# Performance work log

Measured on AMD Instinct MI355X. Metric: run time of the kernel, lower is better.

Reference implementation:

```python
import jax, jax.numpy as jnp
import numpy as np

N = 50000
IN_C, HID_C, OUT_C = 128, 64, 32
E = 800000
NEG_SLOPE = 0.2


def setup_inputs() -> dict:
    key = jax.random.key(0)
    ks = jax.random.split(key, 8)
    x = jax.random.normal(ks[0], (N, IN_C), dtype=jnp.float32)
    edge_index = jax.random.randint(ks[1], (2, E), 0, N, dtype=jnp.int64)
    # GATConv params (heads=1): lin weight, att_src/att_dst vectors, bias
    sc = 1.0 / np.sqrt(IN_C)
    W = jax.random.uniform(ks[2], (IN_C, HID_C), jnp.float32, -sc, sc)
    att_src = jax.random.normal(ks[3], (HID_C,), jnp.float32) * (1.0 / np.sqrt(HID_C))
    att_dst = jax.random.normal(ks[4], (HID_C,), jnp.float32) * (1.0 / np.sqrt(HID_C))
    bias_conv = jnp.zeros((HID_C,), jnp.float32)
    sl = 1.0 / np.sqrt(HID_C)
    W_lin = jax.random.uniform(ks[5], (HID_C, OUT_C), jnp.float32, -sl, sl)
    b_lin = jax.random.uniform(ks[6], (OUT_C,), jnp.float32, -sl, sl)
    return {"x": x, "edge_index": edge_index, "W": W, "att_src": att_src,
            "att_dst": att_dst, "bias_conv": bias_conv, "W_lin": W_lin, "b_lin": b_lin}


def reference(x, edge_index, W, att_src, att_dst, bias_conv, W_lin, b_lin):
    n = x.shape[0]
    h = x @ W  # [N, HID]
    # add self-loops (PyG GATConv default add_self_loops=True)
    loop = jnp.arange(n, dtype=edge_index.dtype)
    src = jnp.concatenate([edge_index[0], loop])  # [E+N]
    dst = jnp.concatenate([edge_index[1], loop])
    a_src = h @ att_src  # [N]
    a_dst = h @ att_dst
    e = jax.nn.leaky_relu(a_src[src] + a_dst[dst], NEG_SLOPE)  # [E+N]
    # segment softmax over incoming edges per destination node
    m = jax.ops.segment_max(e, dst, num_segments=n)
    e = jnp.exp(e - m[dst])
    denom = jax.ops.segment_sum(e, dst, num_segments=n)
    alpha = e / (denom[dst] + 1e-16)
    msg = alpha[:, None] * h[src]  # [E+N, HID]
    out = jax.ops.segment_sum(msg, dst, num_segments=n) + bias_conv
    out = jax.nn.relu(out)
    return out @ W_lin + b_lin
```

## Files before the change

kernel.cpp:

```cpp
#include <hip/hip_runtime.h>
#include <hip/hip_bf16.h>

#define IN_C  128
#define HID_C 64
#define OUT_C 32
#define NEG_SLOPE 0.2f
#define EPB1    4096
#define BUCKETW 64
#define RCAP    1536
#define NBKT    1024
#define CSTRIDE 16
#define XS_LD   136

typedef short bf16x8 __attribute__((ext_vector_type(8)));
typedef float f32x4  __attribute__((ext_vector_type(4)));

__device__ __forceinline__ unsigned short f2bf(float f) {
    __hip_bfloat16 h = __float2bfloat16(f);
    return *(unsigned short*)&h;
}
__device__ __forceinline__ float bflo(unsigned int u) {
    return __uint_as_float(u << 16);
}
__device__ __forceinline__ float bfhi(unsigned int u) {
    return __uint_as_float(u & 0xffff0000u);
}

__global__ __launch_bounds__(512) void gemm_bin1_kernel(
    const float* __restrict__ x, const float* __restrict__ W,
    const float* __restrict__ att_src, const float* __restrict__ att_dst,
    __hip_bfloat16* __restrict__ hb,
    float* __restrict__ a_src, float* __restrict__ a_dst,
    const int* __restrict__ ei, int E,
    int* __restrict__ bcur, unsigned* __restrict__ bucketbuf,
    int ngemm, int n_nodes)
{
    __shared__ __align__(16) unsigned char smem[52224];
    const int t = threadIdx.x;

    if ((int)blockIdx.x < ngemm) {
        unsigned short* xs = (unsigned short*)smem;
        unsigned short* wt = (unsigned short*)(smem + 34816);
        const int wv   = t >> 6;
        const int lane = t & 63;
        const int m16  = lane & 15;
        const int quad = lane >> 4;
        const int node0 = blockIdx.x * 128;
        const int nrows = min(128, n_nodes - node0);

        {
            const float4* xg = (const float4*)(x + (long)node0 * IN_C);
#pragma unroll
            for (int i = t; i < 4096; i += 512) {
                const int row = i >> 5;
                const int c4  = i & 31;
                float4 v = (row < nrows) ? xg[i] : make_float4(0.f, 0.f, 0.f, 0.f);
                ushort4 u;
                u.x = f2bf(v.x); u.y = f2bf(v.y);
                u.z = f2bf(v.z); u.w = f2bf(v.w);
                *(ushort4*)(xs + row * XS_LD + c4 * 4) = u;
            }
        }
        {
#pragma unroll
            for (int i = t; i < 2048; i += 512) {
                const int k  = i >> 4;
                const int n0 = (i & 15) * 4;
                const float4 v = *(const float4*)(W + k * HID_C + n0);
                wt[(n0 + 0) * XS_LD + k] = f2bf(v.x);
                wt[(n0 + 1) * XS_LD + k] = f2bf(v.y);
                wt[(n0 + 2) * XS_LD + k] = f2bf(v.z);
                wt[(n0 + 3) * XS_LD + k] = f2bf(v.w);
            }
        }
        __syncthreads();

        const int myrow0 = wv * 16;
        bf16x8 A[4];
#pragma unroll
        for (int k0 = 0; k0 < 4; ++k0)
            A[k0] = *(const bf16x8*)(xs + (myrow0 + m16) * XS_LD + k0 * 32 + quad * 8);

        f32x4 C[4];
#pragma unroll
        for (int c = 0; c < 4; ++c) {
            C[c] = (f32x4){0.f, 0.f, 0.f, 0.f};
#pragma unroll
            for (int k0 = 0; k0 < 4; ++k0) {
                const bf16x8 B = *(const bf16x8*)(wt + (c * 16 + m16) * XS_LD + k0 * 32 + quad * 8);
                C[c] = __builtin_amdgcn_mfma_f32_16x16x32_bf16(A[k0], B, C[c], 0, 0, 0);
            }
        }

#pragma unroll
        for (int c = 0; c < 4; ++c) {
#pragma unroll
            for (int r = 0; r < 4; ++r)
                xs[(myrow0 + quad * 4 + r) * XS_LD + c * 16 + m16] = f2bf(C[c][r]);
        }

        {
            float ps[4] = {0.f, 0.f, 0.f, 0.f};
            float pd[4] = {0.f, 0.f, 0.f, 0.f};
#pragma unroll
            for (int c = 0; c < 4; ++c) {
                const float av = att_src[c * 16 + m16];
                const float dv = att_dst[c * 16 + m16];
#pragma unroll
                for (int r = 0; r < 4; ++r) {
                    ps[r] = fmaf(C[c][r], av, ps[r]);
                    pd[r] = fmaf(C[c][r], dv, pd[r]);
                }
            }
#pragma unroll
            for (int off = 1; off <= 8; off <<= 1) {
#pragma unroll
                for (int r = 0; r < 4; ++r) {
                    ps[r] += __shfl_xor(ps[r], off, 64);
                    pd[r] += __shfl_xor(pd[r], off, 64);
                }
            }
            if (m16 == 0) {
#pragma unroll
                for (int r = 0; r < 4; ++r) {
                    const int row = myrow0 + quad * 4 + r;
                    if (row < nrows) {
                        a_src[node0 + row] = ps[r];
                        a_dst[node0 + row] = pd[r];
                    }
                }
            }
        }
        __syncthreads();

        {
#pragma unroll
            for (int i = t; i < 1024; i += 512) {
                const int row = i >> 3;
                const int c8  = (i & 7) * 8;
                if (row < nrows) {
                    const uint4 v = *(const uint4*)(xs + row * XS_LD + c8);
                    *(uint4*)((unsigned short*)hb + (long)(node0 + row) * HID_C + c8) = v;
                }
            }
        }
    } else {
        unsigned* stage = (unsigned*)smem;
        int* excl = (int*)(smem + 16384);
        int* cur  = (int*)(smem + 20480);
        int* gpos = (int*)(smem + 24576);
        int* wsum = (int*)(smem + 28672);

        const int base = (blockIdx.x - ngemm) * EPB1;
        const int nedge = min(EPB1, E - base);
        const int lane = t & 63, wv = t >> 6;

        for (int i = t; i < NBKT; i += 512) excl[i] = 0;
        __syncthreads();

        for (int i = t; i < nedge; i += 512)
            atomicAdd(&excl[ei[E + base + i] >> 6], 1);
        __syncthreads();

        {
            const int b0 = t * 2;
            const int c0 = excl[b0], c1 = excl[b0 + 1];
            const int tsum = c0 + c1;
            int incl = tsum;
#pragma unroll
            for (int off = 1; off <= 32; off <<= 1) {
                int u = __shfl_up(incl, off, 64);
                if (lane >= off) incl += u;
            }
            if (lane == 63) wsum[wv] = incl;
            __syncthreads();
            int wbase = 0;
#pragma unroll
            for (int w = 0; w < 8; ++w) wbase += (w < wv) ? wsum[w] : 0;
            int run = wbase + (incl - tsum);
            excl[b0]     = run; cur[b0]     = run; run += c0;
            excl[b0 + 1] = run; cur[b0 + 1] = run;
        }
        __syncthreads();

        for (int i = t; i < nedge; i += 512) {
            const int s = ei[base + i];
            const int d = ei[E + base + i];
            const int b = d >> 6;
            const int pos = atomicAdd(&cur[b], 1);
            stage[pos] = (unsigned)s | ((unsigned)(d & 63) << 16)
                         | ((unsigned)b << 22);
        }
        __syncthreads();

        for (int b = t; b < NBKT; b += 512) {
            const int c = cur[b] - excl[b];
            gpos[b] = (c > 0) ? atomicAdd(&bcur[b * CSTRIDE], c) : 0;
        }
        __syncthreads();

        for (int i = t; i < nedge; i += 512) {
            const unsigned r = stage[i];
            const int b = r >> 22;
            const int dp = gpos[b] + (i - excl[b]);
            if (dp < RCAP) bucketbuf[(long)b * RCAP + dp] = r & 0x3FFFFFu;
        }
    }
}

__global__ __launch_bounds__(512) void bucket_agg_kernel(
    const unsigned* __restrict__ bucketbuf, const int* __restrict__ bcursor,
    const __hip_bfloat16* __restrict__ hb,
    const float* __restrict__ a_src, const float* __restrict__ a_dst,
    const float* __restrict__ bias_conv,
    const float* __restrict__ W_lin, const float* __restrict__ b_lin,
    float* __restrict__ out, int n_nodes)
{
    __shared__ unsigned srtL[RCAP];
    __shared__ int cntd[BUCKETW];
    __shared__ int rp[BUCKETW + 1];
    __shared__ int curd[BUCKETW];

    const int t  = threadIdx.x;
    const int q  = blockIdx.x;
    const int d0 = q * BUCKETW;
    const int dmax = min(BUCKETW, n_nodes - d0);
    const int tot  = min(bcursor[q * CSTRIDE], RCAP);
    const int wv = t >> 6, lane = t & 63, g8 = lane >> 3, l = lane & 7;

    if (t < BUCKETW) cntd[t] = 0;
    __syncthreads();

    const unsigned* gsrc = bucketbuf + (long)q * RCAP;

    const int i0 = t, i1 = t + 512, i2 = t + 1024;
    const bool v0 = i0 < tot, v1 = i1 < tot, v2 = i2 < tot;
    const unsigned rr0 = v0 ? gsrc[i0] : 0u;
    const unsigned rr1 = v1 ? gsrc[i1] : 0u;
    const unsigned rr2 = v2 ? gsrc[i2] : 0u;

    if (v0) atomicAdd(&cntd[(rr0 >> 16) & 63], 1);
    if (v1) atomicAdd(&cntd[(rr1 >> 16) & 63], 1);
    if (v2) atomicAdd(&cntd[(rr2 >> 16) & 63], 1);
    __syncthreads();

    if (t < 64) {
        int c = cntd[t], incl = c;
#pragma unroll
        for (int off = 1; off <= 32; off <<= 1) {
            int u = __shfl_up(incl, off, 64);
            if (t >= off) incl += u;
        }
        rp[t] = incl - c;
        curd[t] = incl - c;
        if (t == 63) rp[64] = incl;
    }
    __syncthreads();

    if (v0) { const int pos = atomicAdd(&curd[(rr0 >> 16) & 63], 1); srtL[pos] = rr0; }
    if (v1) { const int pos = atomicAdd(&curd[(rr1 >> 16) & 63], 1); srtL[pos] = rr1; }
    if (v2) { const int pos = atomicAdd(&curd[(rr2 >> 16) & 63], 1); srtL[pos] = rr2; }
    __syncthreads();

    float Wr[8][4];
#pragma unroll
    for (int kc = 0; kc < 8; ++kc)
#pragma unroll
        for (int kj = 0; kj < 4; ++kj)
            Wr[kc][kj] = W_lin[(l * 8 + kc) * OUT_C + g8 * 4 + kj];
    float biasR[8];
#pragma unroll
    for (int kc = 0; kc < 8; ++kc) biasR[kc] = bias_conv[l * 8 + kc];
    float blinR[4];
#pragma unroll
    for (int kj = 0; kj < 4; ++kj) blinR[kj] = b_lin[g8 * 4 + kj];

    const unsigned short* hbs = (const unsigned short*)hb;

    for (int dloc = wv; dloc < dmax; dloc += 8) {
        const int d = d0 + dloc;
        const float ad = a_dst[d];
        float A[8] = {0.f,0.f,0.f,0.f,0.f,0.f,0.f,0.f};
        float den = 0.f;
        if (g8 == 0) {
            float e = a_src[d] + ad;
            e = (e >= 0.f) ? e : NEG_SLOPE * e;
            const float ws = __expf(e);
            const uint4 hv = *(const uint4*)(hbs + (long)d * HID_C + l * 8);
            den = ws;
            A[0] = ws * bflo(hv.x); A[1] = ws * bfhi(hv.x);
            A[2] = ws * bflo(hv.y); A[3] = ws * bfhi(hv.y);
            A[4] = ws * bflo(hv.z); A[5] = ws * bfhi(hv.z);
            A[6] = ws * bflo(hv.w); A[7] = ws * bfhi(hv.w);
        }
        const int beg = rp[dloc], fin = rp[dloc + 1];
        for (int j = beg + g8; j < fin; j += 16) {
            const int  j1   = j + 8;
            const bool has1 = j1 < fin;
            const unsigned r0 = srtL[j];
            const unsigned r1 = srtL[has1 ? j1 : j];
            const int   s0 = r0 & 0xFFFF;
            const int   s1 = r1 & 0xFFFF;
            const float as0 = a_src[s0];
            const float as1 = a_src[s1];
            const uint4 h0 = *(const uint4*)(hbs + (long)s0 * HID_C + l * 8);
            const uint4 h1 = *(const uint4*)(hbs + (long)s1 * HID_C + l * 8);
            float e0 = as0 + ad; e0 = (e0 >= 0.f) ? e0 : NEG_SLOPE * e0;
            float e1 = as1 + ad; e1 = (e1 >= 0.f) ? e1 : NEG_SLOPE * e1;
            const float w0 = __expf(e0);
            const float w1 = has1 ? __expf(e1) : 0.f;
            den += w0 + w1;
            A[0] = fmaf(w0, bflo(h0.x), A[0]); A[1] = fmaf(w0, bfhi(h0.x), A[1]);
            A[2] = fmaf(w0, bflo(h0.y), A[2]); A[3] = fmaf(w0, bfhi(h0.y), A[3]);
            A[4] = fmaf(w0, bflo(h0.z), A[4]); A[5] = fmaf(w0, bfhi(h0.z), A[5]);
            A[6] = fmaf(w0, bflo(h0.w), A[6]); A[7] = fmaf(w0, bfhi(h0.w), A[7]);
            A[0] = fmaf(w1, bflo(h1.x), A[0]); A[1] = fmaf(w1, bfhi(h1.x), A[1]);
            A[2] = fmaf(w1, bflo(h1.y), A[2]); A[3] = fmaf(w1, bfhi(h1.y), A[3]);
            A[4] = fmaf(w1, bflo(h1.z), A[4]); A[5] = fmaf(w1, bfhi(h1.z), A[5]);
            A[6] = fmaf(w1, bflo(h1.w), A[6]); A[7] = fmaf(w1, bfhi(h1.w), A[7]);
        }
#pragma unroll
        for (int off = 8; off <= 32; off <<= 1) {
#pragma unroll
            for (int k = 0; k < 8; ++k) A[k] += __shfl_xor(A[k], off, 64);
            den += __shfl_xor(den, off, 64);
        }
        const float rd = 1.0f / (den + 1e-16f);
        float p0 = 0.f, p1 = 0.f, p2 = 0.f, p3 = 0.f;
#pragma unroll
        for (int kc = 0; kc < 8; ++kc) {
            float vv = fmaf(A[kc], rd, biasR[kc]);
            vv = vv > 0.f ? vv : 0.f;
            p0 = fmaf(vv, Wr[kc][0], p0);
            p1 = fmaf(vv, Wr[kc][1], p1);
            p2 = fmaf(vv, Wr[kc][2], p2);
            p3 = fmaf(vv, Wr[kc][3], p3);
        }
#pragma unroll
        for (int off = 1; off <= 4; off <<= 1) {
            p0 += __shfl_xor(p0, off, 64);
            p1 += __shfl_xor(p1, off, 64);
            p2 += __shfl_xor(p2, off, 64);
            p3 += __shfl_xor(p3, off, 64);
        }
        if (l == 0) {
            float4 o = make_float4(p0 + blinR[0], p1 + blinR[1],
                                   p2 + blinR[2], p3 + blinR[3]);
            *(float4*)(out + (long)d * OUT_C + g8 * 4) = o;
        }
    }
}

extern "C" void kernel_launch(void* const* d_in, const int* in_sizes, int n_in,
                              void* d_out, int out_size, void* d_ws, size_t ws_size,
                              hipStream_t stream) {
    const float* x         = (const float*)d_in[0];
    const int*   ei        = (const int*)d_in[1];
    const float* W         = (const float*)d_in[2];
    const float* att_src   = (const float*)d_in[3];
    const float* att_dst   = (const float*)d_in[4];
    const float* bias_conv = (const float*)d_in[5];
    const float* W_lin     = (const float*)d_in[6];
    const float* b_lin     = (const float*)d_in[7];
    float*       out       = (float*)d_out;

    const int n_nodes = in_sizes[0] / IN_C;
    const int E       = in_sizes[1] / 2;
    const int B1   = (E + EPB1 - 1) / EPB1;
    const int Q    = (n_nodes + BUCKETW - 1) / BUCKETW;
    const int NG   = (n_nodes + 127) / 128;

    __hip_bfloat16* hb = (__hip_bfloat16*)d_ws;
    float* a_src   = (float*)(hb + (long)n_nodes * HID_C);
    float* a_dst   = a_src + n_nodes;
    int*   bcur    = (int*)(a_dst + n_nodes);
    unsigned* bucketbuf = (unsigned*)(bcur + (long)Q * CSTRIDE);

    hipMemsetAsync(bcur, 0, (size_t)Q * CSTRIDE * sizeof(int), stream);

    gemm_bin1_kernel<<<NG + B1, 512, 0, stream>>>(
        x, W, att_src, att_dst, hb, a_src, a_dst,
        ei, E, bcur, bucketbuf, NG, n_nodes);

    bucket_agg_kernel<<<Q, 512, 0, stream>>>(
        bucketbuf, bcur, hb, a_src, a_dst,
        bias_conv, W_lin, b_lin, out, n_nodes);
}
```

Before: 150.5 us.

## Fuse GEMM, binning and aggregation into one persistent kernel with grid barrier

Merges the two kernels into a single persistent kernel of 512 blocks. The blocks loop over GEMM and edge-binning work units, meet at a software grid barrier, then loop over aggregation buckets. Buckets now span 98 nodes instead of 64, giving 512 buckets, and each bucket record stores the full destination id. This removes a kernel launch and the gap between kernels. In exchange it relies on all 512 blocks being resident at once for the spin barrier, which includes a guard-break that could silently proceed, and it uses integer division by 98.

```diff
diff --git a/kernel.cpp b/kernel.cpp
--- a/kernel.cpp
+++ b/kernel.cpp
@@ -6,11 +6,12 @@
 #define OUT_C 32
 #define NEG_SLOPE 0.2f
 #define EPB1    4096
-#define BUCKETW 64
-#define RCAP    1536
-#define NBKT    1024
+#define BUCKETW 98
+#define RCAP    2048
+#define NBKT    512
 #define CSTRIDE 16
 #define XS_LD   136
+#define NBLK    512
 
 typedef short bf16x8 __attribute__((ext_vector_type(8)));
 typedef float f32x4  __attribute__((ext_vector_type(4)));
@@ -26,327 +27,355 @@
     return __uint_as_float(u & 0xffff0000u);
 }
 
-__global__ __launch_bounds__(512) void gemm_bin1_kernel(
+__device__ __forceinline__ void grid_barrier(int* ctr, int nb) {
+    __syncthreads();
+    __threadfence();
+    if (threadIdx.x == 0) {
+        atomicAdd(ctr, 1);
+        int guard = 0;
+        while (__hip_atomic_load(ctr, __ATOMIC_RELAXED,
+                                 __HIP_MEMORY_SCOPE_AGENT) < nb) {
+            __builtin_amdgcn_s_sleep(8);
+            if (++guard > (1 << 20)) break;
+        }
+    }
+    __syncthreads();
+    __threadfence();
+}
+
+__global__ __launch_bounds__(512, 4) void gat_fused(
     const float* __restrict__ x, const float* __restrict__ W,
     const float* __restrict__ att_src, const float* __restrict__ att_dst,
     __hip_bfloat16* __restrict__ hb,
     float* __restrict__ a_src, float* __restrict__ a_dst,
     const int* __restrict__ ei, int E,
-    int* __restrict__ bcur, unsigned* __restrict__ bucketbuf,
-    int ngemm, int n_nodes)
+    int* __restrict__ bar, int* __restrict__ bcur,
+    unsigned* __restrict__ bucketbuf,
+    const float* __restrict__ bias_conv,
+    const float* __restrict__ W_lin, const float* __restrict__ b_lin,
+    float* __restrict__ out,
+    int ngemm, int nbin, int nreg, int n_nodes)
 {
     __shared__ __align__(16) unsigned char smem[52224];
-    const int t = threadIdx.x;
-
-    if ((int)blockIdx.x < ngemm) {
-        unsigned short* xs = (unsigned short*)smem;
-        unsigned short* wt = (unsigned short*)(smem + 34816);
-        const int wv   = t >> 6;
-        const int lane = t & 63;
-        const int m16  = lane & 15;
-        const int quad = lane >> 4;
-        const int node0 = blockIdx.x * 128;
-        const int nrows = min(128, n_nodes - node0);
-
-        {
-            const float4* xg = (const float4*)(x + (long)node0 * IN_C);
-#pragma unroll
-            for (int i = t; i < 4096; i += 512) {
-                const int row = i >> 5;
-                const int c4  = i & 31;
-                float4 v = (row < nrows) ? xg[i] : make_float4(0.f, 0.f, 0.f, 0.f);
-                ushort4 u;
-                u.x = f2bf(v.x); u.y = f2bf(v.y);
-                u.z = f2bf(v.z); u.w = f2bf(v.w);
-                *(ushort4*)(xs + row * XS_LD + c4 * 4) = u;
-            }
-        }
-        {
-#pragma unroll
-            for (int i = t; i < 2048; i += 512) {
-                const int k  = i >> 4;
-                const int n0 = (i & 15) * 4;
-                const float4 v = *(const float4*)(W + k * HID_C + n0);
-                wt[(n0 + 0) * XS_LD + k] = f2bf(v.x);
-                wt[(n0 + 1) * XS_LD + k] = f2bf(v.y);
-                wt[(n0 + 2) * XS_LD + k] = f2bf(v.z);
-                wt[(n0 + 3) * XS_LD + k] = f2bf(v.w);
-            }
-        }
-        __syncthreads();
-
-        const int myrow0 = wv * 16;
-        bf16x8 A[4];
-#pragma unroll
-        for (int k0 = 0; k0 < 4; ++k0)
-            A[k0] = *(const bf16x8*)(xs + (myrow0 + m16) * XS_LD + k0 * 32 + quad * 8);
-
-        f32x4 C[4];
-#pragma unroll
-        for (int c = 0; c < 4; ++c) {
-            C[c] = (f32x4){0.f, 0.f, 0.f, 0.f};
-#pragma unroll
-            for (int k0 = 0; k0 < 4; ++k0) {
-                const bf16x8 B = *(const bf16x8*)(wt + (c * 16 + m16) * XS_LD + k0 * 32 + quad * 8);
-                C[c] = __builtin_amdgcn_mfma_f32_16x16x32_bf16(A[k0], B, C[c], 0, 0, 0);
-            }
-        }
-
-#pragma unroll
-        for (int c = 0; c < 4; ++c) {
-#pragma unroll
-            for (int r = 0; r < 4; ++r)
-                xs[(myrow0 + quad * 4 + r) * XS_LD + c * 16 + m16] = f2bf(C[c][r]);
-        }
-
-        {
-            float ps[4] = {0.f, 0.f, 0.f, 0.f};
-            float pd[4] = {0.f, 0.f, 0.f, 0.f};
+    const int t   = threadIdx.x;
+    const int bid = blockIdx.x;
+
+    for (int u = bid; u < ngemm + nbin; u += NBLK) {
+        if (u < ngemm) {
+            unsigned short* xs = (unsigned short*)smem;
+            unsigned short* wt = (unsigned short*)(smem + 34816);
+            const int wv   = t >> 6;
+            const int lane = t & 63;
+            const int m16  = lane & 15;
+            const int quad = lane >> 4;
+            const int node0 = u * 128;
+            const int nrows = min(128, n_nodes - node0);
+
+            __syncthreads();
+
+            {
+                const float4* xg = (const float4*)(x + (long)node0 * IN_C);
+#pragma unroll
+                for (int i = t; i < 4096; i += 512) {
+                    const int row = i >> 5;
+                    const int c4  = i & 31;
+                    float4 v = (row < nrows) ? xg[i] : make_float4(0.f, 0.f, 0.f, 0.f);
+                    ushort4 uu;
+                    uu.x = f2bf(v.x); uu.y = f2bf(v.y);
+                    uu.z = f2bf(v.z); uu.w = f2bf(v.w);
+                    *(ushort4*)(xs + row * XS_LD + c4 * 4) = uu;
+                }
+            }
+            {
+#pragma unroll
+                for (int i = t; i < 2048; i += 512) {
+                    const int k  = i >> 4;
+                    const int n0 = (i & 15) * 4;
+                    const float4 v = *(const float4*)(W + k * HID_C + n0);
+                    wt[(n0 + 0) * XS_LD + k] = f2bf(v.x);
+                    wt[(n0 + 1) * XS_LD + k] = f2bf(v.y);
+                    wt[(n0 + 2) * XS_LD + k] = f2bf(v.z);
+                    wt[(n0 + 3) * XS_LD + k] = f2bf(v.w);
+                }
+            }
+            __syncthreads();
+
+            const int myrow0 = wv * 16;
+            bf16x8 A[4];
+#pragma unroll
+            for (int k0 = 0; k0 < 4; ++k0)
+                A[k0] = *(const bf16x8*)(xs + (myrow0 + m16) * XS_LD + k0 * 32 + quad * 8);
+
+            f32x4 C[4];
 #pragma unroll
             for (int c = 0; c < 4; ++c) {
-                const float av = att_src[c * 16 + m16];
-                const float dv = att_dst[c * 16 + m16];
-#pragma unroll
-                for (int r = 0; r < 4; ++r) {
-                    ps[r] = fmaf(C[c][r], av, ps[r]);
-                    pd[r] = fmaf(C[c][r], dv, pd[r]);
-                }
-            }
-#pragma unroll
-            for (int off = 1; off <= 8; off <<= 1) {
-#pragma unroll
-                for (int r = 0; r < 4; ++r) {
-                    ps[r] += __shfl_xor(ps[r], off, 64);
-                    pd[r] += __shfl_xor(pd[r], off, 64);
-                }
-            }
-            if (m16 == 0) {
-#pragma unroll
-                for (int r = 0; r < 4; ++r) {
-                    const int row = myrow0 + quad * 4 + r;
+                C[c] = (f32x4){0.f, 0.f, 0.f, 0.f};
+#pragma unroll
+                for (int k0 = 0; k0 < 4; ++k0) {
+                    const bf16x8 B = *(const bf16x8*)(wt + (c * 16 + m16) * XS_LD + k0 * 32 + quad * 8);
+                    C[c] = __builtin_amdgcn_mfma_f32_16x16x32_bf16(A[k0], B, C[c], 0, 0, 0);
+                }
+            }
+
+#pragma unroll
+            for (int c = 0; c < 4; ++c) {
+#pragma unroll
+                for (int r = 0; r < 4; ++r)
+                    xs[(myrow0 + quad * 4 + r) * XS_LD + c * 16 + m16] = f2bf(C[c][r]);
+            }
+
+            {
+                float ps[4] = {0.f, 0.f, 0.f, 0.f};
+                float pd[4] = {0.f, 0.f, 0.f, 0.f};
+#pragma unroll
+                for (int c = 0; c < 4; ++c) {
+                    const float av = att_src[c * 16 + m16];
+                    const float dv = att_dst[c * 16 + m16];
+#pragma unroll
+                    for (int r = 0; r < 4; ++r) {
+                        ps[r] = fmaf(C[c][r], av, ps[r]);
+                        pd[r] = fmaf(C[c][r], dv, pd[r]);
+                    }
+                }
+#pragma unroll
+                for (int off = 1; off <= 8; off <<= 1) {
+#pragma unroll
+                    for (int r = 0; r < 4; ++r) {
+                        ps[r] += __shfl_xor(ps[r], off, 64);
+                        pd[r] += __shfl_xor(pd[r], off, 64);
+                    }
+                }
+                if (m16 == 0) {
+#pragma unroll
+                    for (int r = 0; r < 4; ++r) {
+                        const int row = myrow0 + quad * 4 + r;
+                        if (row < nrows) {
+                            a_src[node0 + row] = ps[r];
+                            a_dst[node0 + row] = pd[r];
+                        }
+                    }
+                }
+            }
+            __syncthreads();
+
+            {
+#pragma unroll
+                for (int i = t; i < 1024; i += 512) {
+                    const int row = i >> 3;
+                    const int c8  = (i & 7) * 8;
                     if (row < nrows) {
-                        a_src[node0 + row] = ps[r];
-                        a_dst[node0 + row] = pd[r];
+                        const uint4 v = *(const uint4*)(xs + row * XS_LD + c8);
+                        *(uint4*)((unsigned short*)hb + (long)(node0 + row) * HID_C + c8) = v;
                     }
                 }
             }
-        }
-        __syncthreads();
-
-        {
-#pragma unroll
-            for (int i = t; i < 1024; i += 512) {
-                const int row = i >> 3;
-                const int c8  = (i & 7) * 8;
-                if (row < nrows) {
-                    const uint4 v = *(const uint4*)(xs + row * XS_LD + c8);
-                    *(uint4*)((unsigned short*)hb + (long)(node0 + row) * HID_C + c8) = v;
-                }
-            }
-        }
-    } else {
-        unsigned* stage = (unsigned*)smem;
-        int* excl = (int*)(smem + 16384);
-        int* cur  = (int*)(smem + 20480);
-        int* gpos = (int*)(smem + 24576);
-        int* wsum = (int*)(smem + 28672);
-
-        const int base = (blockIdx.x - ngemm) * EPB1;
-        const int nedge = min(EPB1, E - base);
-        const int lane = t & 63, wv = t >> 6;
-
-        for (int i = t; i < NBKT; i += 512) excl[i] = 0;
-        __syncthreads();
-
-        for (int i = t; i < nedge; i += 512)
-            atomicAdd(&excl[ei[E + base + i] >> 6], 1);
-        __syncthreads();
-
-        {
-            const int b0 = t * 2;
-            const int c0 = excl[b0], c1 = excl[b0 + 1];
-            const int tsum = c0 + c1;
-            int incl = tsum;
-#pragma unroll
-            for (int off = 1; off <= 32; off <<= 1) {
-                int u = __shfl_up(incl, off, 64);
-                if (lane >= off) incl += u;
-            }
-            if (lane == 63) wsum[wv] = incl;
-            __syncthreads();
-            int wbase = 0;
-#pragma unroll
-            for (int w = 0; w < 8; ++w) wbase += (w < wv) ? wsum[w] : 0;
-            int run = wbase + (incl - tsum);
-            excl[b0]     = run; cur[b0]     = run; run += c0;
-            excl[b0 + 1] = run; cur[b0 + 1] = run;
-        }
-        __syncthreads();
-
-        for (int i = t; i < nedge; i += 512) {
-            const int s = ei[base + i];
-            const int d = ei[E + base + i];
-            const int b = d >> 6;
-            const int pos = atomicAdd(&cur[b], 1);
-            stage[pos] = (unsigned)s | ((unsigned)(d & 63) << 16)
-                         | ((unsigned)b << 22);
-        }
-        __syncthreads();
-
-        for (int b = t; b < NBKT; b += 512) {
-            const int c = cur[b] - excl[b];
-            gpos[b] = (c > 0) ? atomicAdd(&bcur[b * CSTRIDE], c) : 0;
-        }
-        __syncthreads();
-
-        for (int i = t; i < nedge; i += 512) {
-            const unsigned r = stage[i];
-            const int b = r >> 22;
-            const int dp = gpos[b] + (i - excl[b]);
-            if (dp < RCAP) bucketbuf[(long)b * RCAP + dp] = r & 0x3FFFFFu;
+        } else {
+            unsigned* stage = (unsigned*)smem;
+            int* excl = (int*)(smem + 16384);
+            int* cur  = (int*)(smem + 18432);
+            int* gpos = (int*)(smem + 20480);
+            int* wsum = (int*)(smem + 22528);
+
+            const int base = (u - ngemm) * EPB1;
+            const int nedge = min(EPB1, E - base);
+            const int lane = t & 63, wv = t >> 6;
+
+            __syncthreads();
+
+            excl[t] = 0;
+            __syncthreads();
+
+            for (int i = t; i < nedge; i += 512)
+                atomicAdd(&excl[(unsigned)ei[E + base + i] / 98u], 1);
+            __syncthreads();
+
+            {
+                const int c = excl[t];
+                int incl = c;
+#pragma unroll
+                for (int off = 1; off <= 32; off <<= 1) {
+                    int uu = __shfl_up(incl, off, 64);
+                    if (lane >= off) incl += uu;
+                }
+                if (lane == 63) wsum[wv] = incl;
+                __syncthreads();
+                int wbase = 0;
+#pragma unroll
+                for (int w = 0; w < 8; ++w) wbase += (w < wv) ? wsum[w] : 0;
+                const int e = wbase + incl - c;
+                excl[t] = e; cur[t] = e;
+            }
+            __syncthreads();
+
+            for (int i = t; i < nedge; i += 512) {
+                const int s = ei[base + i];
+                const int d = ei[E + base + i];
+                const int b = (unsigned)d / 98u;
+                const int pos = atomicAdd(&cur[b], 1);
+                stage[pos] = (unsigned)s | ((unsigned)d << 16);
+            }
+            __syncthreads();
+
+            {
+                const int c = cur[t] - excl[t];
+                gpos[t] = (c > 0) ? atomicAdd(&bcur[t * CSTRIDE], c) : 0;
+            }
+            __syncthreads();
+
+            for (int i = t; i < nedge; i += 512) {
+                const unsigned r = stage[i];
+                const int b = (r >> 16) / 98u;
+                const int dp = gpos[b] + (i - excl[b]);
+                if (dp < RCAP) bucketbuf[(long)b * RCAP + dp] = r;
+            }
         }
     }
-}
-
-__global__ __launch_bounds__(512) void bucket_agg_kernel(
-    const unsigned* __restrict__ bucketbuf, const int* __restrict__ bcursor,
-    const __hip_bfloat16* __restrict__ hb,
-    const float* __restrict__ a_src, const float* __restrict__ a_dst,
-    const float* __restrict__ bias_conv,
-    const float* __restrict__ W_lin, const float* __restrict__ b_lin,
-    float* __restrict__ out, int n_nodes)
-{
-    __shared__ unsigned srtL[RCAP];
-    __shared__ int cntd[BUCKETW];
-    __shared__ int rp[BUCKETW + 1];
-    __shared__ int curd[BUCKETW];
-
-    const int t  = threadIdx.x;
-    const int q  = blockIdx.x;
-    const int d0 = q * BUCKETW;
-    const int dmax = min(BUCKETW, n_nodes - d0);
-    const int tot  = min(bcursor[q * CSTRIDE], RCAP);
-    const int wv = t >> 6, lane = t & 63, g8 = lane >> 3, l = lane & 7;
-
-    if (t < BUCKETW) cntd[t] = 0;
-    __syncthreads();
-
-    const unsigned* gsrc = bucketbuf + (long)q * RCAP;
-
-    const int i0 = t, i1 = t + 512, i2 = t + 1024;
-    const bool v0 = i0 < tot, v1 = i1 < tot, v2 = i2 < tot;
-    const unsigned rr0 = v0 ? gsrc[i0] : 0u;
-    const unsigned rr1 = v1 ? gsrc[i1] : 0u;
-    const unsigned rr2 = v2 ? gsrc[i2] : 0u;
-
-    if (v0) atomicAdd(&cntd[(rr0 >> 16) & 63], 1);
-    if (v1) atomicAdd(&cntd[(rr1 >> 16) & 63], 1);
-    if (v2) atomicAdd(&cntd[(rr2 >> 16) & 63], 1);
-    __syncthreads();
-
-    if (t < 64) {
-        int c = cntd[t], incl = c;
-#pragma unroll
-        for (int off = 1; off <= 32; off <<= 1) {
-            int u = __shfl_up(incl, off, 64);
-            if (t >= off) incl += u;
+
+    grid_barrier(bar, NBLK);
+
+    unsigned* srtL = (unsigned*)smem;
+    int* cntd = (int*)(smem + 8192);
+    int* rp   = (int*)(smem + 8584);
+    int* curd = (int*)(smem + 8980);
+
+    for (int q = bid; q < nreg; q += NBLK) {
+        const int d0 = q * BUCKETW;
+        const int dmax = min(BUCKETW, n_nodes - d0);
+        const int tot  = min(bcur[q * CSTRIDE], RCAP);
+        const int wv = t >> 6, lane = t & 63, g8 = lane >> 3, l = lane & 7;
+
+        __syncthreads();
+        if (t < BUCKETW) cntd[t] = 0;
+        __syncthreads();
+
+        const unsigned* gsrc = bucketbuf + (long)q * RCAP;
+
+        const int i0 = t, i1 = t + 512, i2 = t + 1024, i3 = t + 1536;
+        const bool v0 = i0 < tot, v1 = i1 < tot, v2 = i2 < tot, v3 = i3 < tot;
+        const unsigned rr0 = v0 ? gsrc[i0] : 0u;
+        const unsigned rr1 = v1 ? gsrc[i1] : 0u;
+        const unsigned rr2 = v2 ? gsrc[i2] : 0u;
+        const unsigned rr3 = v3 ? gsrc[i3] : 0u;
+
+        if (v0) atomicAdd(&cntd[(int)(rr0 >> 16) - d0], 1);
+        if (v1) atomicAdd(&cntd[(int)(rr1 >> 16) - d0], 1);
+        if (v2) atomicAdd(&cntd[(int)(rr2 >> 16) - d0], 1);
+        if (v3) atomicAdd(&cntd[(int)(rr3 >> 16) - d0], 1);
+        __syncthreads();
+
+        if (t < 64) {
+            int c = cntd[t], incl = c;
+#pragma unroll
+            for (int off = 1; off <= 32; off <<= 1) {
+                int uu = __shfl_up(incl, off, 64);
+                if (t >= off) incl += uu;
+            }
+            rp[t] = incl - c;
+            curd[t] = incl - c;
+            if (t == 63) rp[64] = incl;
         }
-        rp[t] = incl - c;
-        curd[t] = incl - c;
-        if (t == 63) rp[64] = incl;
-    }
-    __syncthreads();
-
-    if (v0) { const int pos = atomicAdd(&curd[(rr0 >> 16) & 63], 1); srtL[pos] = rr0; }
-    if (v1) { const int pos = atomicAdd(&curd[(rr1 >> 16) & 63], 1); srtL[pos] = rr1; }
-    if (v2) { const int pos = atomicAdd(&curd[(rr2 >> 16) & 63], 1); srtL[pos] = rr2; }
-    __syncthreads();
-
-    float Wr[8][4];
-#pragma unroll
-    for (int kc = 0; kc < 8; ++kc)
-#pragma unroll
-        for (int kj = 0; kj < 4; ++kj)
-            Wr[kc][kj] = W_lin[(l * 8 + kc) * OUT_C + g8 * 4 + kj];
-    float biasR[8];
-#pragma unroll
-    for (int kc = 0; kc < 8; ++kc) biasR[kc] = bias_conv[l * 8 + kc];
-    float blinR[4];
-#pragma unroll
-    for (int kj = 0; kj < 4; ++kj) blinR[kj] = b_lin[g8 * 4 + kj];
-
-    const unsigned short* hbs = (const unsigned short*)hb;
-
-    for (int dloc = wv; dloc < dmax; dloc += 8) {
-        const int d = d0 + dloc;
-        const float ad = a_dst[d];
-        float A[8] = {0.f,0.f,0.f,0.f,0.f,0.f,0.f,0.f};
-        float den = 0.f;
-        if (g8 == 0) {
-            float e = a_src[d] + ad;
-            e = (e >= 0.f) ? e : NEG_SLOPE * e;
-            const float ws = __expf(e);
-            const uint4 hv = *(const uint4*)(hbs + (long)d * HID_C + l * 8);
-            den = ws;
-            A[0] = ws * bflo(hv.x); A[1] = ws * bfhi(hv.x);
-            A[2] = ws * bflo(hv.y); A[3] = ws * bfhi(hv.y);
-            A[4] = ws * bflo(hv.z); A[5] = ws * bfhi(hv.z);
-            A[6] = ws * bflo(hv.w); A[7] = ws * bfhi(hv.w);
+        __syncthreads();
+        if (t == 0) {
+            int run = rp[64];
+            for (int k = 64; k < BUCKETW; ++k) {
+                rp[k] = run; curd[k] = run; run += cntd[k];
+            }
+            rp[BUCKETW] = run;
         }
-        const int beg = rp[dloc], fin = rp[dloc + 1];
-        for (int j = beg + g8; j < fin; j += 16) {
-            const int  j1   = j + 8;
-            const bool has1 = j1 < fin;
-            const unsigned r0 = srtL[j];
-            const unsigned r1 = srtL[has1 ? j1 : j];
-            const int   s0 = r0 & 0xFFFF;
-            const int   s1 = r1 & 0xFFFF;
-            const float as0 = a_src[s0];
-            const float as1 = a_src[s1];
-            const uint4 h0 = *(const uint4*)(hbs + (long)s0 * HID_C + l * 8);
-            const uint4 h1 = *(const uint4*)(hbs + (long)s1 * HID_C + l * 8);
-            float e0 = as0 + ad; e0 = (e0 >= 0.f) ? e0 : NEG_SLOPE * e0;
-            float e1 = as1 + ad; e1 = (e1 >= 0.f) ? e1 : NEG_SLOPE * e1;
-            const float w0 = __expf(e0);
-            const float w1 = has1 ? __expf(e1) : 0.f;
-            den += w0 + w1;
-            A[0] = fmaf(w0, bflo(h0.x), A[0]); A[1] = fmaf(w0, bfhi(h0.x), A[1]);
-            A[2] = fmaf(w0, bflo(h0.y), A[2]); A[3] = fmaf(w0, bfhi(h0.y), A[3]);
-            A[4] = fmaf(w0, bflo(h0.z), A[4]); A[5] = fmaf(w0, bfhi(h0.z), A[5]);
-            A[6] = fmaf(w0, bflo(h0.w), A[6]); A[7] = fmaf(w0, bfhi(h0.w), A[7]);
-            A[0] = fmaf(w1, bflo(h1.x), A[0]); A[1] = fmaf(w1, bfhi(h1.x), A[1]);
-            A[2] = fmaf(w1, bflo(h1.y), A[2]); A[3] = fmaf(w1, bfhi(h1.y), A[3]);
-            A[4] = fmaf(w1, bflo(h1.z), A[4]); A[5] = fmaf(w1, bfhi(h1.z), A[5]);
-            A[6] = fmaf(w1, bflo(h1.w), A[6]); A[7] = fmaf(w1, bfhi(h1.w), A[7]);
-        }
-#pragma unroll
-        for (int off = 8; off <= 32; off <<= 1) {
-#pragma unroll
-            for (int k = 0; k < 8; ++k) A[k] += __shfl_xor(A[k], off, 64);
-            den += __shfl_xor(den, off, 64);
-        }
-        const float rd = 1.0f / (den + 1e-16f);
-        float p0 = 0.f, p1 = 0.f, p2 = 0.f, p3 = 0.f;
-#pragma unroll
-        for (int kc = 0; kc < 8; ++kc) {
-            float vv = fmaf(A[kc], rd, biasR[kc]);
-            vv = vv > 0.f ? vv : 0.f;
-            p0 = fmaf(vv, Wr[kc][0], p0);
-            p1 = fmaf(vv, Wr[kc][1], p1);
-            p2 = fmaf(vv, Wr[kc][2], p2);
-            p3 = fmaf(vv, Wr[kc][3], p3);
-        }
-#pragma unroll
-        for (int off = 1; off <= 4; off <<= 1) {
-            p0 += __shfl_xor(p0, off, 64);
-            p1 += __shfl_xor(p1, off, 64);
-            p2 += __shfl_xor(p2, off, 64);
-            p3 += __shfl_xor(p3, off, 64);
-        }
-        if (l == 0) {
-            float4 o = make_float4(p0 + blinR[0], p1 + blinR[1],
-                                   p2 + blinR[2], p3 + blinR[3]);
-            *(float4*)(out + (long)d * OUT_C + g8 * 4) = o;
+        __syncthreads();
+
+        if (v0) { const int p = atomicAdd(&curd[(int)(rr0 >> 16) - d0], 1); srtL[p] = rr0; }
+        if (v1) { const int p = atomicAdd(&curd[(int)(rr1 >> 16) - d0], 1); srtL[p] = rr1; }
+        if (v2) { const int p = atomicAdd(&curd[(int)(rr2 >> 16) - d0], 1); srtL[p] = rr2; }
+        if (v3) { const int p = atomicAdd(&curd[(int)(rr3 >> 16) - d0], 1); srtL[p] = rr3; }
+        __syncthreads();
+
+        float Wr[8][4];
+#pragma unroll
+        for (int kc = 0; kc < 8; ++kc)
+#pragma unroll
+            for (int kj = 0; kj < 4; ++kj)
+                Wr[kc][kj] = W_lin[(l * 8 + kc) * OUT_C + g8 * 4 + kj];
+        float biasR[8];
+#pragma unroll
+        for (int kc = 0; kc < 8; ++kc) biasR[kc] = bias_conv[l * 8 + kc];
+        float blinR[4];
+#pragma unroll
+        for (int kj = 0; kj < 4; ++kj) blinR[kj] = b_lin[g8 * 4 + kj];
+
+        const unsigned short* hbs = (const unsigned short*)hb;
+
+        for (int dloc = wv; dloc < dmax; dloc += 8) {
+            const int d = d0 + dloc;
+            const float ad = a_dst[d];
+            float A[8] = {0.f,0.f,0.f,0.f,0.f,0.f,0.f,0.f};
+            float den = 0.f;
+            if (g8 == 0) {
+                float e = a_src[d] + ad;
+                e = (e >= 0.f) ? e : NEG_SLOPE * e;
+                const float ws = __expf(e);
+                const uint4 hv = *(const uint4*)(hbs + (long)d * HID_C + l * 8);
+                den = ws;
+                A[0] = ws * bflo(hv.x); A[1] = ws * bfhi(hv.x);
+                A[2] = ws * bflo(hv.y); A[3] = ws * bfhi(hv.y);
+                A[4] = ws * bflo(hv.z); A[5] = ws * bfhi(hv.z);
+                A[6] = ws * bflo(hv.w); A[7] = ws * bfhi(hv.w);
+            }
+            const int beg = rp[dloc], fin = rp[dloc + 1];
+            for (int j = beg + g8; j < fin; j += 16) {
+                const int  j1   = j + 8;
+                const bool has1 = j1 < fin;
+                const unsigned r0 = srtL[j];
+                const unsigned r1 = srtL[has1 ? j1 : j];
+                const int   s0 = r0 & 0xFFFF;
+                const int   s1 = r1 & 0xFFFF;
+                const float as0 = a_src[s0];
+                const float as1 = a_src[s1];
+                const uint4 h0 = *(const uint4*)(hbs + (long)s0 * HID_C + l * 8);
+                const uint4 h1 = *(const uint4*)(hbs + (long)s1 * HID_C + l * 8);
+                float e0 = as0 + ad; e0 = (e0 >= 0.f) ? e0 : NEG_SLOPE * e0;
+                float e1 = as1 + ad; e1 = (e1 >= 0.f) ? e1 : NEG_SLOPE * e1;
+                const float w0 = __expf(e0);
+                const float w1 = has1 ? __expf(e1) : 0.f;
+                den += w0 + w1;
+                A[0] = fmaf(w0, bflo(h0.x), A[0]); A[1] = fmaf(w0, bfhi(h0.x), A[1]);
+                A[2] = fmaf(w0, bflo(h0.y), A[2]); A[3] = fmaf(w0, bfhi(h0.y), A[3]);
+                A[4] = fmaf(w0, bflo(h0.z), A[4]); A[5] = fmaf(w0, bfhi(h0.z), A[5]);
+                A[6] = fmaf(w0, bflo(h0.w), A[6]); A[7] = fmaf(w0, bfhi(h0.w), A[7]);
+                A[0] = fmaf(w1, bflo(h1.x), A[0]); A[1] = fmaf(w1, bfhi(h1.x), A[1]);
+                A[2] = fmaf(w1, bflo(h1.y), A[2]); A[3] = fmaf(w1, bfhi(h1.y), A[3]);
+                A[4] = fmaf(w1, bflo(h1.z), A[4]); A[5] = fmaf(w1, bfhi(h1.z), A[5]);
+                A[6] = fmaf(w1, bflo(h1.w), A[6]); A[7] = fmaf(w1, bfhi(h1.w), A[7]);
+            }
+#pragma unroll
+            for (int off = 8; off <= 32; off <<= 1) {
+#pragma unroll
+                for (int k = 0; k < 8; ++k) A[k] += __shfl_xor(A[k], off, 64);
+                den += __shfl_xor(den, off, 64);
+            }
+            const float rd = 1.0f / (den + 1e-16f);
+            float p0 = 0.f, p1 = 0.f, p2 = 0.f, p3 = 0.f;
+#pragma unroll
+            for (int kc = 0; kc < 8; ++kc) {
+                float vv = fmaf(A[kc], rd, biasR[kc]);
+                vv = vv > 0.f ? vv : 0.f;
+                p0 = fmaf(vv, Wr[kc][0], p0);
+                p1 = fmaf(vv, Wr[kc][1], p1);
+                p2 = fmaf(vv, Wr[kc][2], p2);
+                p3 = fmaf(vv, Wr[kc][3], p3);
+            }
+#pragma unroll
+            for (int off = 1; off <= 4; off <<= 1) {
+                p0 += __shfl_xor(p0, off, 64);
+                p1 += __shfl_xor(p1, off, 64);
+                p2 += __shfl_xor(p2, off, 64);
+                p3 += __shfl_xor(p3, off, 64);
+            }
+            if (l == 0) {
+                float4 o = make_float4(p0 + blinR[0], p1 + blinR[1],
+                                       p2 + blinR[2], p3 + blinR[3]);
+                *(float4*)(out + (long)d * OUT_C + g8 * 4) = o;
+            }
         }
     }
 }
@@ -364,25 +393,25 @@
     const float* b_lin     = (const float*)d_in[7];
     float*       out       = (float*)d_out;
 
-    const int n_nodes = in_sizes[0] / IN_C;
-    const int E       = in_sizes[1] / 2;
-    const int B1   = (E + EPB1 - 1) / EPB1;
-    const int Q    = (n_nodes + BUCKETW - 1) / BUCKETW;
-    const int NG   = (n_nodes + 127) / 128;
+    int n_nodes = in_sizes[0] / IN_C;
+    int E       = in_sizes[1] / 2;
+    int nbin    = (E + EPB1 - 1) / EPB1;
+    int nreg    = (n_nodes + BUCKETW - 1) / BUCKETW;
+    int ngemm   = (n_nodes + 127) / 128;
 
     __hip_bfloat16* hb = (__hip_bfloat16*)d_ws;
     float* a_src   = (float*)(hb + (long)n_nodes * HID_C);
     float* a_dst   = a_src + n_nodes;
-    int*   bcur    = (int*)(a_dst + n_nodes);
-    unsigned* bucketbuf = (unsigned*)(bcur + (long)Q * CSTRIDE);
-
-    hipMemsetAsync(bcur, 0, (size_t)Q * CSTRIDE * sizeof(int), stream);
-
-    gemm_bin1_kernel<<<NG + B1, 512, 0, stream>>>(
+    int*   bar     = (int*)(a_dst + n_nodes);
+    int*   bcur    = bar + 16;
+    unsigned* bucketbuf = (unsigned*)(bcur + (long)nreg * CSTRIDE);
+
+    hipMemsetAsync(bar, 0, (size_t)(16 + (long)nreg * CSTRIDE) * sizeof(int),
+                   stream);
+
+    gat_fused<<<NBLK, 512, 0, stream>>>(
         x, W, att_src, att_dst, hb, a_src, a_dst,
-        ei, E, bcur, bucketbuf, NG, n_nodes);
-
-    bucket_agg_kernel<<<Q, 512, 0, stream>>>(
-        bucketbuf, bcur, hb, a_src, a_dst,
-        bias_conv, W_lin, b_lin, out, n_nodes);
-}
+        ei, E, bar, bcur, bucketbuf,
+        bias_conv, W_lin, b_lin, out,
+        ngemm, nbin, nreg, n_nodes);
+}
```

New measurement: 319.0 us. 2.12x slower.

## Precompute per-edge attention weights in a separate kernel before aggregation

Applied to the files above, without the earlier changes.

Adds a weight_kernel that computes exp(leaky_relu(a_src+a_dst)) for every bucketed edge and stores it in a new global buffer. The aggregation kernel then loads these weights, sorts them into shared memory alongside the edge records, and no longer does the a_src gather or the exp in its inner loop. This takes the dependent scalar gather and the transcendental off the critical path of the aggregation loop. In exchange it adds a kernel launch, an extra global write and read of the weights, and more shared memory per block, which may lower occupancy.

```diff
diff --git a/kernel.cpp b/kernel.cpp
--- a/kernel.cpp
+++ b/kernel.cpp
@@ -208,8 +208,37 @@
     }
 }
 
+__global__ __launch_bounds__(512) void weight_kernel(
+    const unsigned* __restrict__ bucketbuf, const int* __restrict__ bcursor,
+    const float* __restrict__ a_src, const float* __restrict__ a_dst,
+    float* __restrict__ wbuf)
+{
+    const int t = threadIdx.x;
+    const int q = blockIdx.x;
+    const int d0 = q * BUCKETW;
+    const int tot = min(bcursor[q * CSTRIDE], RCAP);
+    const unsigned* src = bucketbuf + (long)q * RCAP;
+    float* wdst = wbuf + (long)q * RCAP;
+
+    const int i0 = t, i1 = t + 512, i2 = t + 1024;
+    const bool v0 = i0 < tot, v1 = i1 < tot, v2 = i2 < tot;
+    const unsigned r0 = v0 ? src[i0] : 0u;
+    const unsigned r1 = v1 ? src[i1] : 0u;
+    const unsigned r2 = v2 ? src[i2] : 0u;
+    const float as0 = v0 ? a_src[r0 & 0xFFFF] : 0.f;
+    const float as1 = v1 ? a_src[r1 & 0xFFFF] : 0.f;
+    const float as2 = v2 ? a_src[r2 & 0xFFFF] : 0.f;
+    const float ad0 = v0 ? a_dst[d0 + ((r0 >> 16) & 63)] : 0.f;
+    const float ad1 = v1 ? a_dst[d0 + ((r1 >> 16) & 63)] : 0.f;
+    const float ad2 = v2 ? a_dst[d0 + ((r2 >> 16) & 63)] : 0.f;
+    if (v0) { float e = as0 + ad0; e = (e >= 0.f) ? e : NEG_SLOPE * e; wdst[i0] = __expf(e); }
+    if (v1) { float e = as1 + ad1; e = (e >= 0.f) ? e : NEG_SLOPE * e; wdst[i1] = __expf(e); }
+    if (v2) { float e = as2 + ad2; e = (e >= 0.f) ? e : NEG_SLOPE * e; wdst[i2] = __expf(e); }
+}
+
 __global__ __launch_bounds__(512) void bucket_agg_kernel(
-    const unsigned* __restrict__ bucketbuf, const int* __restrict__ bcursor,
+    const unsigned* __restrict__ bucketbuf, const float* __restrict__ wbuf,
+    const int* __restrict__ bcursor,
     const __hip_bfloat16* __restrict__ hb,
     const float* __restrict__ a_src, const float* __restrict__ a_dst,
     const float* __restrict__ bias_conv,
@@ -217,6 +246,7 @@
     float* __restrict__ out, int n_nodes)
 {
     __shared__ unsigned srtL[RCAP];
+    __shared__ float    srtW[RCAP];
     __shared__ int cntd[BUCKETW];
     __shared__ int rp[BUCKETW + 1];
     __shared__ int curd[BUCKETW];
@@ -232,12 +262,16 @@
     __syncthreads();
 
     const unsigned* gsrc = bucketbuf + (long)q * RCAP;
+    const float*    wsrc = wbuf + (long)q * RCAP;
 
     const int i0 = t, i1 = t + 512, i2 = t + 1024;
     const bool v0 = i0 < tot, v1 = i1 < tot, v2 = i2 < tot;
     const unsigned rr0 = v0 ? gsrc[i0] : 0u;
     const unsigned rr1 = v1 ? gsrc[i1] : 0u;
     const unsigned rr2 = v2 ? gsrc[i2] : 0u;
+    const float    ww0 = v0 ? wsrc[i0] : 0.f;
+    const float    ww1 = v1 ? wsrc[i1] : 0.f;
+    const float    ww2 = v2 ? wsrc[i2] : 0.f;
 
     if (v0) atomicAdd(&cntd[(rr0 >> 16) & 63], 1);
     if (v1) atomicAdd(&cntd[(rr1 >> 16) & 63], 1);
@@ -257,9 +291,9 @@
     }
     __syncthreads();
 
-    if (v0) { const int pos = atomicAdd(&curd[(rr0 >> 16) & 63], 1); srtL[pos] = rr0; }
-    if (v1) { const int pos = atomicAdd(&curd[(rr1 >> 16) & 63], 1); srtL[pos] = rr1; }
-    if (v2) { const int pos = atomicAdd(&curd[(rr2 >> 16) & 63], 1); srtL[pos] = rr2; }
+    if (v0) { const int p = atomicAdd(&curd[(rr0 >> 16) & 63], 1); srtL[p] = rr0; srtW[p] = ww0; }
+    if (v1) { const int p = atomicAdd(&curd[(rr1 >> 16) & 63], 1); srtL[p] = rr1; srtW[p] = ww1; }
+    if (v2) { const int p = atomicAdd(&curd[(rr2 >> 16) & 63], 1); srtL[p] = rr2; srtW[p] = ww2; }
     __syncthreads();
 
     float Wr[8][4];
@@ -279,11 +313,10 @@
 
     for (int dloc = wv; dloc < dmax; dloc += 8) {
         const int d = d0 + dloc;
-        const float ad = a_dst[d];
         float A[8] = {0.f,0.f,0.f,0.f,0.f,0.f,0.f,0.f};
         float den = 0.f;
         if (g8 == 0) {
-            float e = a_src[d] + ad;
+            float e = a_src[d] + a_dst[d];
             e = (e >= 0.f) ? e : NEG_SLOPE * e;
             const float ws = __expf(e);
             const uint4 hv = *(const uint4*)(hbs + (long)d * HID_C + l * 8);
@@ -297,18 +330,15 @@
         for (int j = beg + g8; j < fin; j += 16) {
             const int  j1   = j + 8;
             const bool has1 = j1 < fin;
+            const int  j1c  = has1 ? j1 : j;
             const unsigned r0 = srtL[j];
-            const unsigned r1 = srtL[has1 ? j1 : j];
+            const unsigned r1 = srtL[j1c];
+            const float w0 = srtW[j];
+            const float w1 = has1 ? srtW[j1c] : 0.f;
             const int   s0 = r0 & 0xFFFF;
             const int   s1 = r1 & 0xFFFF;
-            const float as0 = a_src[s0];
-            const float as1 = a_src[s1];
             const uint4 h0 = *(const uint4*)(hbs + (long)s0 * HID_C + l * 8);
             const uint4 h1 = *(const uint4*)(hbs + (long)s1 * HID_C + l * 8);
-            float e0 = as0 + ad; e0 = (e0 >= 0.f) ? e0 : NEG_SLOPE * e0;
-            float e1 = as1 + ad; e1 = (e1 >= 0.f) ? e1 : NEG_SLOPE * e1;
-            const float w0 = __expf(e0);
-            const float w1 = has1 ? __expf(e1) : 0.f;
             den += w0 + w1;
             A[0] = fmaf(w0, bflo(h0.x), A[0]); A[1] = fmaf(w0, bfhi(h0.x), A[1]);
             A[2] = fmaf(w0, bflo(h0.y), A[2]); A[3] = fmaf(w0, bfhi(h0.y), A[3]);
@@ -375,6 +405,7 @@
     float* a_dst   = a_src + n_nodes;
     int*   bcur    = (int*)(a_dst + n_nodes);
     unsigned* bucketbuf = (unsigned*)(bcur + (long)Q * CSTRIDE);
+    float* wbuf    = (float*)(bucketbuf + (long)Q * RCAP);
 
     hipMemsetAsync(bcur, 0, (size_t)Q * CSTRIDE * sizeof(int), stream);
 
@@ -382,7 +413,10 @@
         x, W, att_src, att_dst, hb, a_src, a_dst,
         ei, E, bcur, bucketbuf, NG, n_nodes);
 
+    weight_kernel<<<Q, 512, 0, stream>>>(
+        bucketbuf, bcur, a_src, a_dst, wbuf);
+
     bucket_agg_kernel<<<Q, 512, 0, stream>>>(
-        bucketbuf, bcur, hb, a_src, a_dst,
+        bucketbuf, wbuf, bcur, hb, a_src, a_dst,
         bias_conv, W_lin, b_lin, out, n_nodes);
 }
```

After: 155.3 us. +3.2%, slower.
